# Performance work log

Measured on AMD Instinct MI355X. Metric: run time of the kernel, lower is better.

## Reference

```python
import jax, jax.numpy as jnp
import numpy as np

N_EMBED = 1024
HEAD_COUNT = 16
HEAD_SIZE = 64  # HEAD_COUNT * HEAD_SIZE == N_EMBED
SEQ = 2048
BATCH = 2


def setup_inputs() -> dict:
    key = jax.random.key(0)
    k_ix, k_q, k_k, k_v, k_p, k_b = jax.random.split(key, 6)
    scale = 1.0 / np.sqrt(N_EMBED)
    inp = {
        "ix": jax.random.normal(k_ix, (BATCH, SEQ, N_EMBED), dtype=jnp.float32),
        # per-head projection weights, stored as x @ W form: [H, C, D]
        "Wq": jax.random.normal(k_q, (HEAD_COUNT, N_EMBED, HEAD_SIZE), dtype=jnp.float32) * scale,
        "Wk": jax.random.normal(k_k, (HEAD_COUNT, N_EMBED, HEAD_SIZE), dtype=jnp.float32) * scale,
        "Wv": jax.random.normal(k_v, (HEAD_COUNT, N_EMBED, HEAD_SIZE), dtype=jnp.float32) * scale,
        # output projection (Linear with bias): y = x @ Wp + bp
        "Wp": jax.random.normal(k_p, (N_EMBED, N_EMBED), dtype=jnp.float32) * scale,
        "bp": jax.random.normal(k_b, (N_EMBED,), dtype=jnp.float32) * scale,
    }
    return inp


def reference(ix, Wq, Wk, Wv, Wp, bp):
    B, T, C = ix.shape
    # per-head projections: [B, H, T, D]
    Q = jnp.einsum("btc,hcd->bhtd", ix, Wq)
    K = jnp.einsum("btc,hcd->bhtd", ix, Wk)
    V = jnp.einsum("btc,hcd->bhtd", ix, Wv)
    # NOTE: faithful to source -- scores are MULTIPLIED by sqrt(C) (C = n_embed)
    scores = jnp.einsum("bhtd,bhsd->bhts", Q, K) * (C ** 0.5)
    causal = jnp.tril(jnp.ones((T, T), dtype=bool))
    scores = jnp.where(causal, scores, -jnp.inf)
    wei = jax.nn.softmax(scores, axis=-1)
    out = jnp.einsum("bhts,bhsd->bhtd", wei, V)
    # concat heads (matches torch.cat over per-head outputs along last dim)
    out = out.transpose(0, 2, 1, 3).reshape(B, T, -1)
    return out @ Wp + bp
```

## Files before the change

### kernel.cpp

```cpp
#include <hip/hip_runtime.h>

#define BATCH 2
#define SEQL  2048
#define NEMB  1024
#define NH    16
#define HD    64
#define MROWS (BATCH*SEQL)

#define QSCALE 46.166241308446828f

typedef short bf16x8 __attribute__((ext_vector_type(8)));
typedef float f32x16 __attribute__((ext_vector_type(16)));

__device__ __forceinline__ unsigned short f2bf(float x) {
    union { float f; unsigned u; } v; v.f = x;
    unsigned r = v.u + 0x7FFFu + ((v.u >> 16) & 1u);
    return (unsigned short)(r >> 16);
}
__device__ __forceinline__ void split_bf16(float x, unsigned short& hi, unsigned short& lo) {
    hi = f2bf(x);
    union { unsigned u; float f; } h; h.u = ((unsigned)hi) << 16;
    lo = f2bf(x - h.f);
}
__device__ __forceinline__ unsigned cvt_pk_bf16(float a, float b) {
    unsigned r;
    asm("v_cvt_pk_bf16_f32 %0, %1, %2" : "=v"(r) : "v"(a), "v"(b));
    return r;
}
__device__ __forceinline__ void plane_swap(unsigned& a, unsigned& b) {
    asm volatile("v_permlane32_swap_b32 %0, %1" : "+v"(a), "+v"(b));
}

__device__ __forceinline__ int slot16(int chunk, int lane) {
    return chunk * 66 + (lane & 31) + 33 * (lane >> 5);
}

__global__ __launch_bounds__(256) void split_convert_kernel(
    const float* __restrict__ src,
    unsigned short* __restrict__ dhi, unsigned short* __restrict__ dlo)
{
    int i = (blockIdx.x * 256 + threadIdx.x) * 4;
    float4 v = *(const float4*)(src + i);
    unsigned short h[4], l[4];
    split_bf16(v.x, h[0], l[0]); split_bf16(v.y, h[1], l[1]);
    split_bf16(v.z, h[2], l[2]); split_bf16(v.w, h[3], l[3]);
    uint2 ph, pl;
    ph.x = h[0] | ((unsigned)h[1] << 16); ph.y = h[2] | ((unsigned)h[3] << 16);
    pl.x = l[0] | ((unsigned)l[1] << 16); pl.y = l[2] | ((unsigned)l[3] << 16);
    *(uint2*)(dhi + i) = ph;
    *(uint2*)(dlo + i) = pl;
}

__global__ __launch_bounds__(256) void transpose_convert_kernel(
    const float* __restrict__ Wq, const float* __restrict__ Wk,
    const float* __restrict__ Wv, const float* __restrict__ Wp,
    unsigned short* __restrict__ qhi, unsigned short* __restrict__ qlo,
    unsigned short* __restrict__ khi, unsigned short* __restrict__ klo,
    unsigned short* __restrict__ vhi, unsigned short* __restrict__ pt)
{
    __shared__ float tile[64][68];
    const int z = blockIdx.z, hb = blockIdx.y, c0 = blockIdx.x * 64;
    const float* src; int rstride; unsigned short* dhi; unsigned short* dlo;
    if (z == 0)      { src = Wq + (size_t)hb * 65536; rstride = 64;   dhi = qhi; dlo = qlo; }
    else if (z == 1) { src = Wk + (size_t)hb * 65536; rstride = 64;   dhi = khi; dlo = klo; }
    else if (z == 2) { src = Wv + (size_t)hb * 65536; rstride = 64;   dhi = vhi; dlo = nullptr; }
    else             { src = Wp + (size_t)hb * 64;    rstride = 1024; dhi = pt;  dlo = nullptr; }
    const int tid = threadIdx.x;
    #pragma unroll
    for (int i = 0; i < 4; ++i) {
        int fidx = i * 256 + tid;
        int r  = fidx >> 4;
        int dq = (fidx & 15) * 4;
        float4 v = *(const float4*)(src + (size_t)(c0 + r) * rstride + dq);
        *(float4*)&tile[r][dq] = v;
    }
    __syncthreads();
    #pragma unroll
    for (int i = 0; i < 4; ++i) {
        int fidx = i * 256 + tid;
        int d  = fidx >> 4;
        int cq = (fidx & 15) * 4;
        size_t base = (size_t)(hb * 64 + d) * 1024 + c0 + cq;
        unsigned short hh[4], ll[4];
        #pragma unroll
        for (int j = 0; j < 4; ++j) split_bf16(tile[cq + j][d], hh[j], ll[j]);
        uint2 ph; ph.x = hh[0] | ((unsigned)hh[1] << 16); ph.y = hh[2] | ((unsigned)hh[3] << 16);
        *(uint2*)(dhi + base) = ph;
        if (dlo) {
            uint2 pl; pl.x = ll[0] | ((unsigned)ll[1] << 16); pl.y = ll[2] | ((unsigned)ll[3] << 16);
            *(uint2*)(dlo + base) = pl;
        }
    }
}

__global__ __launch_bounds__(256, 2) void qkv_gemm(
    const unsigned short* __restrict__ Ahi, const unsigned short* __restrict__ Alo,
    const unsigned short* __restrict__ Bq_hi, const unsigned short* __restrict__ Bq_lo,
    const unsigned short* __restrict__ Bk_hi, const unsigned short* __restrict__ Bk_lo,
    const unsigned short* __restrict__ Bv_hi,
    unsigned short* __restrict__ Qhi, unsigned short* __restrict__ Qlo,
    unsigned short* __restrict__ Khi, unsigned short* __restrict__ Klo,
    unsigned short* __restrict__ Vt)
{
    __shared__ unsigned short smem[2][4][4224];

    const int z = blockIdx.z;
    const bool split = (z < 2);
    const unsigned short* __restrict__ Bhi = (z == 0) ? Bq_hi : (z == 1) ? Bk_hi : Bv_hi;
    const unsigned short* __restrict__ Blo = (z == 0) ? Bq_lo : Bk_lo;
    unsigned short* __restrict__ Ohi = (z == 0) ? Qhi : Khi;
    unsigned short* __restrict__ Olo = (z == 0) ? Qlo : Klo;
    const float oscale = (z == 0) ? QSCALE : 1.0f;

    const int m0 = blockIdx.x * 128;
    const int n0 = blockIdx.y * 128;
    const int tid  = threadIdx.x;
    const int wid  = tid >> 6, lane = tid & 63;
    const int wr   = wid >> 1, wc = wid & 1;

    int roff_[2], slot_[2];
    #pragma unroll
    for (int q = 0; q < 2; ++q) {
        int f   = q * 256 + tid;
        int row = f >> 2;
        int k8  = (f & 3) * 8;
        roff_[q] = row * 1024 + k8;
        slot_[q] = slot16((row >> 5) * 2 + (k8 >> 4), (row & 31) + 32 * ((k8 >> 3) & 1)) * 8;
    }
    const unsigned short* __restrict__ Ah = Ahi + (size_t)m0 * 1024;
    const unsigned short* __restrict__ Bh = Bhi + (size_t)n0 * 1024;
    const unsigned short* __restrict__ Al = split ? Alo + (size_t)m0 * 1024 : Ahi;
    const unsigned short* __restrict__ Bl = split ? Blo + (size_t)n0 * 1024 : Bhi;

    bf16x8 pah[2], pbh[2], pal[2], pbl[2];

    #define LOADT(KK)  do { _Pragma("unroll")                                   \
        for (int q = 0; q < 2; ++q) {                                           \
            pah[q] = *(const bf16x8*)(Ah + roff_[q] + (KK));                    \
            pbh[q] = *(const bf16x8*)(Bh + roff_[q] + (KK));                    \
            if (split) {                                                        \
                pal[q] = *(const bf16x8*)(Al + roff_[q] + (KK));                \
                pbl[q] = *(const bf16x8*)(Bl + roff_[q] + (KK));                \
            }                                                                   \
        } } while (0)

    #define WRITET(NB) do { _Pragma("unroll")                                   \
        for (int q = 0; q < 2; ++q) {                                           \
            *(bf16x8*)(&smem[NB][0][slot_[q]]) = pah[q];                        \
            *(bf16x8*)(&smem[NB][1][slot_[q]]) = pbh[q];                        \
            if (split) {                                                        \
                *(bf16x8*)(&smem[NB][2][slot_[q]]) = pal[q];                    \
                *(bf16x8*)(&smem[NB][3][slot_[q]]) = pbl[q];                    \
            }                                                                   \
        } } while (0)

    f32x16 acc[2][2] = {};

    LOADT(0);
    WRITET(0);
    LOADT(32);

    for (int t = 0; t < 32; ++t) {
        __syncthreads();
        if (t + 1 < 32) {
            WRITET((t + 1) & 1);
            if (t + 2 < 32) LOADT((t + 2) * 32);
        }
        const int cb = t & 1;
        const unsigned short* a_hi = smem[cb][0];
        const unsigned short* b_hi = smem[cb][1];
        const unsigned short* a_lo = smem[cb][2];
        const unsigned short* b_lo = smem[cb][3];

        #pragma unroll
        for (int kch = 0; kch < 2; ++kch) {
            bf16x8 ah[2], bh_[2];
            #pragma unroll
            for (int mt = 0; mt < 2; ++mt)
                ah[mt] = *(const bf16x8*)(a_hi + slot16((2 * wr + mt) * 2 + kch, lane) * 8);
            #pragma unroll
            for (int nt = 0; nt < 2; ++nt)
                bh_[nt] = *(const bf16x8*)(b_hi + slot16((2 * wc + nt) * 2 + kch, lane) * 8);
            if (split) {
                bf16x8 al[2], bl[2];
                #pragma unroll
                for (int mt = 0; mt < 2; ++mt)
                    al[mt] = *(const bf16x8*)(a_lo + slot16((2 * wr + mt) * 2 + kch, lane) * 8);
                #pragma unroll
                for (int nt = 0; nt < 2; ++nt)
                    bl[nt] = *(const bf16x8*)(b_lo + slot16((2 * wc + nt) * 2 + kch, lane) * 8);
                #pragma unroll
                for (int mt = 0; mt < 2; ++mt)
                    #pragma unroll
                    for (int nt = 0; nt < 2; ++nt) {
                        acc[mt][nt] = __builtin_amdgcn_mfma_f32_32x32x16_bf16(ah[mt], bh_[nt], acc[mt][nt], 0, 0, 0);
                        acc[mt][nt] = __builtin_amdgcn_mfma_f32_32x32x16_bf16(ah[mt], bl[nt],  acc[mt][nt], 0, 0, 0);
                        acc[mt][nt] = __builtin_amdgcn_mfma_f32_32x32x16_bf16(al[mt], bh_[nt], acc[mt][nt], 0, 0, 0);
                    }
            } else {
                #pragma unroll
                for (int mt = 0; mt < 2; ++mt)
                    #pragma unroll
                    for (int nt = 0; nt < 2; ++nt)
                        acc[mt][nt] = __builtin_amdgcn_mfma_f32_32x32x16_bf16(bh_[nt], ah[mt], acc[mt][nt], 0, 0, 0);
            }
        }
    }
    #undef LOADT
    #undef WRITET

    #pragma unroll
    for (int mt = 0; mt < 2; ++mt) {
        #pragma unroll
        for (int nt = 0; nt < 2; ++nt) {
            if (z == 2) {
                const int mcol = m0 + wr * 64 + mt * 32 + (lane & 31);
                const int bb = mcol >> 11, tt = mcol & (SEQL - 1);
                #pragma unroll
                for (int r = 0; r < 16; ++r) {
                    int nrow = n0 + wc * 64 + nt * 32 + (r & 3) + 8 * (r >> 2) + 4 * (lane >> 5);
                    int head = nrow >> 6, dd = nrow & 63;
                    Vt[((size_t)(bb * NH + head) * HD + dd) * SEQL + tt] = f2bf(acc[mt][nt][r]);
                }
            } else {
                const int ncol = n0 + wc * 64 + nt * 32 + (lane & 31);
                const int head = ncol >> 6, d = ncol & 63;
                #pragma unroll
                for (int r = 0; r < 16; ++r) {
                    int mrow = m0 + wr * 64 + mt * 32 + (r & 3) + 8 * (r >> 2) + 4 * (lane >> 5);
                    int bb = mrow >> 11, t = mrow & (SEQL - 1);
                    size_t idx = ((size_t)(bb * NH + head) * SEQL + t) * HD + d;
                    float v = acc[mt][nt][r] * oscale;
                    unsigned short hi = f2bf(v);
                    Ohi[idx] = hi;
                    union { unsigned u; float f; } hf; hf.u = ((unsigned)hi) << 16;
                    Olo[idx] = f2bf(v - hf.f);
                }
            }
        }
    }
}

__global__ __launch_bounds__(256) void attn_mfma_kernel(
    const unsigned short* __restrict__ Qhi, const unsigned short* __restrict__ Qlo,
    const unsigned short* __restrict__ Khi, const unsigned short* __restrict__ Klo,
    const unsigned short* __restrict__ Vt,
    unsigned short* __restrict__ AO)
{
    __shared__ unsigned short smem[2][2][4224];

    const int bid = blockIdx.x;
    const int xcd = bid & 7;
    const int idx = bid >> 3;
    const int bh  = xcd * 4 + (idx & 3);
    const int g   = 15 - (idx >> 2);

    const int tid  = threadIdx.x;
    const int wid  = tid >> 6;
    const int lane = tid & 63;
    const int ln   = lane & 31;
    const int h    = lane >> 5;

    const int qb_idx = g * 4 + wid;
    const int qb     = qb_idx * 32;
    const int qglob  = qb + ln;
    const int my_nt  = (qb_idx >> 1) + 1;
    const int tmax   = 2 * g + 2;

    const unsigned short* __restrict__ Qbh = Qhi + (size_t)bh * SEQL * HD;
    const unsigned short* __restrict__ Qbl = Qlo + (size_t)bh * SEQL * HD;
    const unsigned short* __restrict__ Kbh = Khi + (size_t)bh * SEQL * HD;
    const unsigned short* __restrict__ Kbl = Klo + (size_t)bh * SEQL * HD;
    const unsigned short* __restrict__ Vtb = Vt  + (size_t)bh * HD * SEQL;

    bf16x8 qhi[4], qlo[4];
    #pragma unroll
    for (int c = 0; c < 4; ++c) {
        qhi[c] = *(const bf16x8*)(Qbh + (size_t)qglob * HD + c * 16 + h * 8);
        qlo[c] = *(const bf16x8*)(Qbl + (size_t)qglob * HD + c * 16 + h * 8);
    }

    int s_[2], d8_[2], ks_[2];
    #pragma unroll
    for (int ff = 0; ff < 2; ++ff) {
        int fidx = ff * 256 + tid;
        s_[ff]  = fidx >> 3;
        d8_[ff] = fidx & 7;
        ks_[ff] = slot16((s_[ff] >> 5) * 4 + (d8_[ff] >> 1),
                         (s_[ff] & 31) + 32 * (d8_[ff] & 1)) * 8;
    }
    const size_t voff = (size_t)ln * SEQL + h * 8;

    bf16x8 kh[2], kl[2];
    #pragma unroll
    for (int ff = 0; ff < 2; ++ff) {
        kh[ff] = *(const bf16x8*)(Kbh + (size_t)s_[ff] * HD + d8_[ff] * 8);
        kl[ff] = *(const bf16x8*)(Kbl + (size_t)s_[ff] * HD + d8_[ff] * 8);
    }
    #pragma unroll
    for (int ff = 0; ff < 2; ++ff) {
        *(bf16x8*)(&smem[0][0][ks_[ff]]) = kh[ff];
        *(bf16x8*)(&smem[0][1][ks_[ff]]) = kl[ff];
    }
    if (tmax > 1) {
        #pragma unroll
        for (int ff = 0; ff < 2; ++ff) {
            kh[ff] = *(const bf16x8*)(Kbh + (size_t)(64 + s_[ff]) * HD + d8_[ff] * 8);
            kl[ff] = *(const bf16x8*)(Kbl + (size_t)(64 + s_[ff]) * HD + d8_[ff] * 8);
        }
    }

    f32x16 oacc[2] = {};
    float m_run = -1e30f, l_run = 0.f;

    for (int t = 0; t < tmax; ++t) {
        __syncthreads();
        const int s0 = t * 64;

        bf16x8 vf[8];
        if (t < my_nt) {
            #pragma unroll
            for (int dt = 0; dt < 2; ++dt)
                #pragma unroll
                for (int sc = 0; sc < 4; ++sc)
                    vf[dt * 4 + sc] = *(const bf16x8*)(
                        Vtb + (size_t)dt * 32 * SEQL + voff + s0 + sc * 16);
        }

        if (t + 1 < tmax) {
            const int nb = (t + 1) & 1;
            #pragma unroll
            for (int ff = 0; ff < 2; ++ff) {
                *(bf16x8*)(&smem[nb][0][ks_[ff]]) = kh[ff];
                *(bf16x8*)(&smem[nb][1][ks_[ff]]) = kl[ff];
            }
            if (t + 2 < tmax) {
                const int s0n = (t + 2) * 64;
                #pragma unroll
                for (int ff = 0; ff < 2; ++ff) {
                    kh[ff] = *(const bf16x8*)(Kbh + (size_t)(s0n + s_[ff]) * HD + d8_[ff] * 8);
                    kl[ff] = *(const bf16x8*)(Kbl + (size_t)(s0n + s_[ff]) * HD + d8_[ff] * 8);
                }
            }
        }

        if (t < my_nt) {
            const int cb = t & 1;
            const bf16x8* khf = (const bf16x8*)&smem[cb][0][0];
            const bf16x8* klf = (const bf16x8*)&smem[cb][1][0];

            f32x16 sacc[2] = {};
            __builtin_amdgcn_s_setprio(1);
            #pragma unroll
            for (int sb = 0; sb < 2; ++sb) {
                #pragma unroll
                for (int c = 0; c < 4; ++c) {
                    bf16x8 ah = khf[slot16(sb * 4 + c, lane)];
                    bf16x8 al = klf[slot16(sb * 4 + c, lane)];
                    sacc[sb] = __builtin_amdgcn_mfma_f32_32x32x16_bf16(ah, qhi[c], sacc[sb], 0, 0, 0);
                    sacc[sb] = __builtin_amdgcn_mfma_f32_32x32x16_bf16(ah, qlo[c], sacc[sb], 0, 0, 0);
                    sacc[sb] = __builtin_amdgcn_mfma_f32_32x32x16_bf16(al, qhi[c], sacc[sb], 0, 0, 0);
                }
            }
            __builtin_amdgcn_s_setprio(0);

            const bool diag = (s0 + 63) > qb;
            float mtile = -1e30f;
            #pragma unroll
            for (int sb = 0; sb < 2; ++sb) {
                #pragma unroll
                for (int r = 0; r < 16; ++r) {
                    int srow = (r & 3) + 8 * (r >> 2) + 4 * h + sb * 32;
                    float x = sacc[sb][r];
                    if (diag && (s0 + srow) > qglob) x = -1e30f;
                    sacc[sb][r] = x;
                    mtile = fmaxf(mtile, x);
                }
            }
            mtile = fmaxf(mtile, __shfl_xor(mtile, 32));

            if (!__all(mtile - m_run <= 11.5f)) {
                const float mnew  = fmaxf(m_run, mtile);
                const float alpha = exp2f(m_run - mnew);
                l_run *= alpha;
                #pragma unroll
                for (int dt = 0; dt < 2; ++dt)
                    #pragma unroll
                    for (int r = 0; r < 16; ++r)
                        oacc[dt][r] *= alpha;
                m_run = mnew;
            }

            float psum = 0.f;
            unsigned pw[2][8];
            #pragma unroll
            for (int sb = 0; sb < 2; ++sb) {
                #pragma unroll
                for (int r2 = 0; r2 < 8; ++r2) {
                    float p0 = exp2f(sacc[sb][2 * r2]     - m_run);
                    float p1 = exp2f(sacc[sb][2 * r2 + 1] - m_run);
                    psum += p0 + p1;
                    pw[sb][r2] = cvt_pk_bf16(p0, p1);
                }
            }
            psum += __shfl_xor(psum, 32);
            l_run += psum;

            bf16x8 pfrag[4];
            #pragma unroll
            for (int sb = 0; sb < 2; ++sb) {
                #pragma unroll
                for (int c = 0; c < 2; ++c) {
                    unsigned u0 = pw[sb][4 * c + 0], u2 = pw[sb][4 * c + 2];
                    unsigned u1 = pw[sb][4 * c + 1], u3 = pw[sb][4 * c + 3];
                    plane_swap(u0, u2);
                    plane_swap(u1, u3);
                    union { unsigned u[4]; bf16x8 v; } cvt;
                    cvt.u[0] = u0; cvt.u[1] = u1; cvt.u[2] = u2; cvt.u[3] = u3;
                    pfrag[sb * 2 + c] = cvt.v;
                }
            }

            __builtin_amdgcn_s_setprio(1);
            #pragma unroll
            for (int dt = 0; dt < 2; ++dt)
                #pragma unroll
                for (int sc = 0; sc < 4; ++sc)
                    oacc[dt] = __builtin_amdgcn_mfma_f32_32x32x16_bf16(
                        vf[dt * 4 + sc], pfrag[sc], oacc[dt], 0, 0, 0);
            __builtin_amdgcn_s_setprio(0);
        }
    }

    const float inv = 1.0f / l_run;
    unsigned short* aop = AO + ((size_t)(bh >> 4) * SEQL + qglob) * NEMB + (bh & 15) * HD;
    #pragma unroll
    for (int dt = 0; dt < 2; ++dt) {
        #pragma unroll
        for (int rg = 0; rg < 4; ++rg) {
            int d0 = dt * 32 + rg * 8 + h * 4;
            uint2 w;
            w.x = cvt_pk_bf16(oacc[dt][rg * 4 + 0] * inv, oacc[dt][rg * 4 + 1] * inv);
            w.y = cvt_pk_bf16(oacc[dt][rg * 4 + 2] * inv, oacc[dt][rg * 4 + 3] * inv);
            *(uint2*)(aop + d0) = w;
        }
    }
}

__global__ __launch_bounds__(256, 2) void out_proj_kernel(
    const unsigned short* __restrict__ A, const unsigned short* __restrict__ B,
    const float* __restrict__ bias, float* __restrict__ out)
{
    __shared__ unsigned short smem[2][2][4224];

    const int m0 = blockIdx.x * 128;
    const int n0 = blockIdx.y * 128;
    const int tid  = threadIdx.x;
    const int wid  = tid >> 6, lane = tid & 63;
    const int wr   = wid >> 1, wc = wid & 1;

    int roff_[2], slot_[2];
    #pragma unroll
    for (int q = 0; q < 2; ++q) {
        int f   = q * 256 + tid;
        int row = f >> 2;
        int k8  = (f & 3) * 8;
        roff_[q] = row * 1024 + k8;
        slot_[q] = slot16((row >> 5) * 2 + (k8 >> 4), (row & 31) + 32 * ((k8 >> 3) & 1)) * 8;
    }
    const unsigned short* __restrict__ Ab = A + (size_t)m0 * 1024;
    const unsigned short* __restrict__ Bb = B + (size_t)n0 * 1024;

    bf16x8 pa[2], pb[2];
    #pragma unroll
    for (int q = 0; q < 2; ++q) {
        pa[q] = *(const bf16x8*)(Ab + roff_[q]);
        pb[q] = *(const bf16x8*)(Bb + roff_[q]);
    }
    #pragma unroll
    for (int q = 0; q < 2; ++q) {
        *(bf16x8*)(&smem[0][0][slot_[q]]) = pa[q];
        *(bf16x8*)(&smem[0][1][slot_[q]]) = pb[q];
    }
    #pragma unroll
    for (int q = 0; q < 2; ++q) {
        pa[q] = *(const bf16x8*)(Ab + roff_[q] + 32);
        pb[q] = *(const bf16x8*)(Bb + roff_[q] + 32);
    }

    f32x16 acc[2][2] = {};

    for (int t = 0; t < 32; ++t) {
        __syncthreads();
        if (t + 1 < 32) {
            const int nb = (t + 1) & 1;
            #pragma unroll
            for (int q = 0; q < 2; ++q) {
                *(bf16x8*)(&smem[nb][0][slot_[q]]) = pa[q];
                *(bf16x8*)(&smem[nb][1][slot_[q]]) = pb[q];
            }
            if (t + 2 < 32) {
                #pragma unroll
                for (int q = 0; q < 2; ++q) {
                    pa[q] = *(const bf16x8*)(Ab + roff_[q] + (t + 2) * 32);
                    pb[q] = *(const bf16x8*)(Bb + roff_[q] + (t + 2) * 32);
                }
            }
        }
        const int cb = t & 1;
        const unsigned short* a_s = smem[cb][0];
        const unsigned short* b_s = smem[cb][1];
        #pragma unroll
        for (int kch = 0; kch < 2; ++kch) {
            bf16x8 ah[2], bh_[2];
            #pragma unroll
            for (int mt = 0; mt < 2; ++mt)
                ah[mt] = *(const bf16x8*)(a_s + slot16((2 * wr + mt) * 2 + kch, lane) * 8);
            #pragma unroll
            for (int nt = 0; nt < 2; ++nt)
                bh_[nt] = *(const bf16x8*)(b_s + slot16((2 * wc + nt) * 2 + kch, lane) * 8);
            #pragma unroll
            for (int mt = 0; mt < 2; ++mt)
                #pragma unroll
                for (int nt = 0; nt < 2; ++nt)
                    acc[mt][nt] = __builtin_amdgcn_mfma_f32_32x32x16_bf16(ah[mt], bh_[nt], acc[mt][nt], 0, 0, 0);
        }
    }

    #pragma unroll
    for (int mt = 0; mt < 2; ++mt) {
        #pragma unroll
        for (int nt = 0; nt < 2; ++nt) {
            const int ncol = n0 + wc * 64 + nt * 32 + (lane & 31);
            const float bv = bias[ncol];
            #pragma unroll
            for (int r = 0; r < 16; ++r) {
                int mrow = m0 + wr * 64 + mt * 32 + (r & 3) + 8 * (r >> 2) + 4 * (lane >> 5);
                out[(size_t)mrow * 1024 + ncol] = acc[mt][nt][r] + bv;
            }
        }
    }
}

extern "C" void kernel_launch(void* const* d_in, const int* in_sizes, int n_in,
                              void* d_out, int out_size, void* d_ws, size_t ws_size,
                              hipStream_t stream)
{
    const float* ix = (const float*)d_in[0];
    const float* Wq = (const float*)d_in[1];
    const float* Wk = (const float*)d_in[2];
    const float* Wv = (const float*)d_in[3];
    const float* Wp = (const float*)d_in[4];
    const float* bp = (const float*)d_in[5];
    float* out = (float*)d_out;

    char* ws = (char*)d_ws;
    #define WSOFF(mb) ((unsigned short*)(ws + (size_t)(mb) * 1024 * 1024))
    unsigned short* ix_hi  = WSOFF(0);
    unsigned short* ix_lo  = WSOFF(8);
    unsigned short* Wqt_hi = WSOFF(16);
    unsigned short* Wqt_lo = WSOFF(18);
    unsigned short* Wkt_hi = WSOFF(20);
    unsigned short* Wkt_lo = WSOFF(22);
    unsigned short* Wvt_hi = WSOFF(24);
    unsigned short* Qhi    = WSOFF(26);
    unsigned short* Qlo    = WSOFF(34);
    unsigned short* Khi    = WSOFF(42);
    unsigned short* Klo    = WSOFF(50);
    unsigned short* Wpt    = WSOFF(58);
    unsigned short* AObf   = WSOFF(0);
    unsigned short* Vt     = (unsigned short*)d_out;
    #undef WSOFF

    split_convert_kernel<<<MROWS * NEMB / 4 / 256, 256, 0, stream>>>(ix, ix_hi, ix_lo);
    transpose_convert_kernel<<<dim3(16, 16, 4), 256, 0, stream>>>(
        Wq, Wk, Wv, Wp, Wqt_hi, Wqt_lo, Wkt_hi, Wkt_lo, Wvt_hi, Wpt);
    qkv_gemm<<<dim3(MROWS / 128, NEMB / 128, 3), 256, 0, stream>>>(
        ix_hi, ix_lo, Wqt_hi, Wqt_lo, Wkt_hi, Wkt_lo, Wvt_hi,
        Qhi, Qlo, Khi, Klo, Vt);
    attn_mfma_kernel<<<512, 256, 0, stream>>>(Qhi, Qlo, Khi, Klo, Vt, AObf);
    out_proj_kernel<<<dim3(MROWS / 128, NEMB / 128), 256, 0, stream>>>(AObf, Wpt, bp, out);
}
```

Baseline: 214.5 us.

## Stage V tiles through shared memory and balance causal work per block

V tiles are now loaded cooperatively into a third shared-memory plane alongside K hi/lo and double-buffered, instead of each wave reading V fragments directly from global memory every iteration. Query block assignment pairs a short and a long causal row (g and 31-g) within each workgroup so all blocks do roughly equal work, replacing the previous grouping of four consecutive query blocks. The masking loop is split from the max reduction, and the row sum uses two partial accumulators. This increases LDS use per block and makes every block run about the same number of K/V iterations.

```diff
diff --git a/kernel.cpp b/kernel.cpp
--- a/kernel.cpp
+++ b/kernel.cpp
@@ -247,13 +247,13 @@
     const unsigned short* __restrict__ Vt,
     unsigned short* __restrict__ AO)
 {
-    __shared__ unsigned short smem[2][2][4224];
+    __shared__ unsigned short smem[2][3][4224];
 
     const int bid = blockIdx.x;
     const int xcd = bid & 7;
     const int idx = bid >> 3;
     const int bh  = xcd * 4 + (idx & 3);
-    const int g   = 15 - (idx >> 2);
+    const int g   = idx >> 2;
 
     const int tid  = threadIdx.x;
     const int wid  = tid >> 6;
@@ -261,11 +261,11 @@
     const int ln   = lane & 31;
     const int h    = lane >> 5;
 
-    const int qb_idx = g * 4 + wid;
+    const int qb_idx = ((wid & 1) ? (31 - g) : g) + ((wid & 2) << 4);
     const int qb     = qb_idx * 32;
     const int qglob  = qb + ln;
     const int my_nt  = (qb_idx >> 1) + 1;
-    const int tmax   = 2 * g + 2;
+    const int tmax   = ((63 - g) >> 1) + 1;
 
     const unsigned short* __restrict__ Qbh = Qhi + (size_t)bh * SEQL * HD;
     const unsigned short* __restrict__ Qbl = Qlo + (size_t)bh * SEQL * HD;
@@ -289,24 +289,26 @@
         ks_[ff] = slot16((s_[ff] >> 5) * 4 + (d8_[ff] >> 1),
                          (s_[ff] & 31) + 32 * (d8_[ff] & 1)) * 8;
     }
-    const size_t voff = (size_t)ln * SEQL + h * 8;
-
-    bf16x8 kh[2], kl[2];
+
+    bf16x8 kh[2], kl[2], vv[2];
     #pragma unroll
     for (int ff = 0; ff < 2; ++ff) {
         kh[ff] = *(const bf16x8*)(Kbh + (size_t)s_[ff] * HD + d8_[ff] * 8);
         kl[ff] = *(const bf16x8*)(Kbl + (size_t)s_[ff] * HD + d8_[ff] * 8);
+        vv[ff] = *(const bf16x8*)(Vtb + (size_t)s_[ff] * SEQL + d8_[ff] * 8);
     }
     #pragma unroll
     for (int ff = 0; ff < 2; ++ff) {
         *(bf16x8*)(&smem[0][0][ks_[ff]]) = kh[ff];
         *(bf16x8*)(&smem[0][1][ks_[ff]]) = kl[ff];
+        *(bf16x8*)(&smem[0][2][ks_[ff]]) = vv[ff];
     }
     if (tmax > 1) {
         #pragma unroll
         for (int ff = 0; ff < 2; ++ff) {
             kh[ff] = *(const bf16x8*)(Kbh + (size_t)(64 + s_[ff]) * HD + d8_[ff] * 8);
             kl[ff] = *(const bf16x8*)(Kbl + (size_t)(64 + s_[ff]) * HD + d8_[ff] * 8);
+            vv[ff] = *(const bf16x8*)(Vtb + (size_t)s_[ff] * SEQL + 64 + d8_[ff] * 8);
         }
     }
 
@@ -315,24 +317,13 @@
 
     for (int t = 0; t < tmax; ++t) {
         __syncthreads();
-        const int s0 = t * 64;
-
-        bf16x8 vf[8];
-        if (t < my_nt) {
-            #pragma unroll
-            for (int dt = 0; dt < 2; ++dt)
-                #pragma unroll
-                for (int sc = 0; sc < 4; ++sc)
-                    vf[dt * 4 + sc] = *(const bf16x8*)(
-                        Vtb + (size_t)dt * 32 * SEQL + voff + s0 + sc * 16);
-        }
-
         if (t + 1 < tmax) {
             const int nb = (t + 1) & 1;
             #pragma unroll
             for (int ff = 0; ff < 2; ++ff) {
                 *(bf16x8*)(&smem[nb][0][ks_[ff]]) = kh[ff];
                 *(bf16x8*)(&smem[nb][1][ks_[ff]]) = kl[ff];
+                *(bf16x8*)(&smem[nb][2][ks_[ff]]) = vv[ff];
             }
             if (t + 2 < tmax) {
                 const int s0n = (t + 2) * 64;
@@ -340,14 +331,17 @@
                 for (int ff = 0; ff < 2; ++ff) {
                     kh[ff] = *(const bf16x8*)(Kbh + (size_t)(s0n + s_[ff]) * HD + d8_[ff] * 8);
                     kl[ff] = *(const bf16x8*)(Kbl + (size_t)(s0n + s_[ff]) * HD + d8_[ff] * 8);
+                    vv[ff] = *(const bf16x8*)(Vtb + (size_t)s_[ff] * SEQL + s0n + d8_[ff] * 8);
                 }
             }
         }
 
         if (t < my_nt) {
             const int cb = t & 1;
+            const int s0 = t * 64;
             const bf16x8* khf = (const bf16x8*)&smem[cb][0][0];
             const bf16x8* klf = (const bf16x8*)&smem[cb][1][0];
+            const bf16x8* vtf = (const bf16x8*)&smem[cb][2][0];
 
             f32x16 sacc[2] = {};
             __builtin_amdgcn_s_setprio(1);
@@ -364,19 +358,22 @@
             }
             __builtin_amdgcn_s_setprio(0);
 
-            const bool diag = (s0 + 63) > qb;
+            if ((s0 + 63) > qb) {
+                #pragma unroll
+                for (int sb = 0; sb < 2; ++sb)
+                    #pragma unroll
+                    for (int r = 0; r < 16; ++r) {
+                        int srow = (r & 3) + 8 * (r >> 2) + 4 * h + sb * 32;
+                        if ((s0 + srow) > qglob) sacc[sb][r] = -1e30f;
+                    }
+            }
+
             float mtile = -1e30f;
             #pragma unroll
-            for (int sb = 0; sb < 2; ++sb) {
-                #pragma unroll
-                for (int r = 0; r < 16; ++r) {
-                    int srow = (r & 3) + 8 * (r >> 2) + 4 * h + sb * 32;
-                    float x = sacc[sb][r];
-                    if (diag && (s0 + srow) > qglob) x = -1e30f;
-                    sacc[sb][r] = x;
-                    mtile = fmaxf(mtile, x);
-                }
-            }
+            for (int sb = 0; sb < 2; ++sb)
+                #pragma unroll
+                for (int r = 0; r < 16; ++r)
+                    mtile = fmaxf(mtile, sacc[sb][r]);
             mtile = fmaxf(mtile, __shfl_xor(mtile, 32));
 
             if (!__all(mtile - m_run <= 11.5f)) {
@@ -391,7 +388,7 @@
                 m_run = mnew;
             }
 
-            float psum = 0.f;
+            float ps0 = 0.f, ps1 = 0.f;
             unsigned pw[2][8];
             #pragma unroll
             for (int sb = 0; sb < 2; ++sb) {
@@ -399,10 +396,11 @@
                 for (int r2 = 0; r2 < 8; ++r2) {
                     float p0 = exp2f(sacc[sb][2 * r2]     - m_run);
                     float p1 = exp2f(sacc[sb][2 * r2 + 1] - m_run);
-                    psum += p0 + p1;
+                    if (sb == 0) ps0 += p0 + p1; else ps1 += p0 + p1;
                     pw[sb][r2] = cvt_pk_bf16(p0, p1);
                 }
             }
+            float psum = ps0 + ps1;
             psum += __shfl_xor(psum, 32);
             l_run += psum;
 
@@ -427,7 +425,7 @@
                 #pragma unroll
                 for (int sc = 0; sc < 4; ++sc)
                     oacc[dt] = __builtin_amdgcn_mfma_f32_32x32x16_bf16(
-                        vf[dt * 4 + sc], pfrag[sc], oacc[dt], 0, 0, 0);
+                        vtf[slot16(dt * 4 + sc, lane)], pfrag[sc], oacc[dt], 0, 0, 0);
             __builtin_amdgcn_s_setprio(0);
         }
     }
```

After: 189.3 us. -11.7%, faster.
